# Performance work log

Measured on AMD Instinct MI355X. Metric: run time of the kernel, lower is better.

The kernel has to match this reference:

```python
import jax, jax.numpy as jnp
import numpy as np

K_TOP = 2          # hardcoded k in MyAttentionFunction
S = 32             # hardcoded spatial size (interpolate to 32x32)
N = S * S          # 1024 patches (patch_size=1, stride=1 unfold)
NEG = jnp.float32(-1e30)  # stand-in for excluding columns from top-k


def setup_inputs() -> dict:
    key = jax.random.key(0)
    k1, k2, k3 = jax.random.split(key, 3)
    C = 4096
    generated = jax.random.normal(k1, (1, C, S, S), dtype=jnp.float32)
    known = jax.random.normal(k2, (1, C, S, S), dtype=jnp.float32)
    mask = jax.random.randint(k3, (1, 1, S, S), 0, 2).astype(jnp.float32)
    return {"generated": generated, "known": known, "mask": mask}


def _forward(generated, known, mask):
    C = generated.shape[1]
    # F.interpolate(mask, (32,32)) nearest, then flatten -> flag in {0,1}, shape (N,)
    flag = jax.image.resize(mask, (1, 1, S, S), method="nearest").reshape(N)
    # MyUnfold(x, 1, 1) == [1, N, C]; drop batch dim of 1.
    P = generated.reshape(C, N).T   # (N, C) patches of `generated`
    Kp = known.reshape(C, N).T      # (N, C) patches of `known`

    norm_p = jnp.sum(P * P, axis=-1)   # (N,)
    norm_k = jnp.sum(Kp * Kp, axis=-1)
    # Full cosine matrices; original restricts rows to flag==1 and columns to
    # flag==0 (cosine0) / flag==1 (cosine1) by extraction; we mask columns with
    # a very negative value so top-k returns the same values with GLOBAL indices
    # (which is exactly what the original reconstructs via nonzero()[indexes]).
    cos0 = (P @ Kp.T) / jnp.sqrt(norm_p[:, None] * norm_k[None, :])  # (N, N)
    cos1 = (P @ P.T) / jnp.sqrt(norm_p[:, None] * norm_p[None, :])
    cos0 = jnp.where(flag[None, :] == 0, cos0, NEG)
    cos1 = jnp.where(flag[None, :] == 1, cos1, NEG)

    w0, i0 = jax.lax.top_k(cos0, K_TOP)  # (N, k) values / global indices
    w1, i1 = jax.lax.top_k(cos1, K_TOP)

    m = flag                      # 1.0 on masked rows
    nm = jnp.sum(m)               # number of masked patches
    # weight means taken only over masked rows, then softmax (original uses
    # .item() + numpy softmax, i.e. detached constants).
    means = jnp.stack(
        [jnp.sum(w0[:, i] * m) / nm for i in range(K_TOP)]
        + [jnp.sum(w1[:, i] * m) / nm for i in range(K_TOP)]
    )
    weights = jax.lax.stop_gradient(jax.nn.softmax(means))  # (2k,)

    # The original builds dense 1024x1024 indicator matrices and bmm's them;
    # each indicator row for a masked patch is one-hot at its retrieved source,
    # so the bmm is just a gather into masked rows. The advanced-indexing quirk
    # ind[mask_idx, src_idx] (nonzero() pairs include a leading 0 column) also
    # unconditionally sets ind[0,0]=1; we reproduce that (set semantics: no
    # double count if row 0 already maps to column 0).
    rtn = jnp.zeros((N, C), dtype=generated.dtype)
    for i in range(2 * K_TOP):
        src = Kp if i < K_TOP else P
        cols = (i0 if i < K_TOP else i1)[:, i % K_TOP]  # (N,) global indices
        out_i = jnp.where(m[:, None] == 1, src[cols], 0.0)  # masked rows only
        dup = 1.0 - ((m[0] == 1) & (cols[0] == 0)).astype(src.dtype)
        out_i = out_i.at[0].add(src[0] * dup)  # spurious ind[0,0]=1 artifact
        rtn = rtn + weights[i] * out_i

    rtn = rtn.reshape(1, S, S, C).transpose(0, 3, 1, 2)  # (1, C, 32, 32)
    return jnp.concatenate([generated, known, rtn], axis=1)


def reference(generated, known, mask):
    return _forward(generated, known, mask)
```

## Files before the change

kernel.cpp:

```cpp
#include <hip/hip_runtime.h>
#include <hip/hip_bf16.h>
#include <math.h>

#define N_TOT 1024
#define C_DIM 4096
#define NEGV  -1e30f

typedef __attribute__((ext_vector_type(8))) short short8;
typedef __attribute__((ext_vector_type(4))) float floatx4;

__device__ inline unsigned short bf16_rn(float v) {
    unsigned int u = __float_as_uint(v);
    unsigned int r = (u + 0x7FFFu + ((u >> 16) & 1u)) >> 16;
    return (unsigned short)r;
}

__global__ __launch_bounds__(256) void split_norms(const float* __restrict__ G,
                                                   const float* __restrict__ Kn,
                                                   unsigned short* __restrict__ Phi,
                                                   unsigned short* __restrict__ Plo,
                                                   unsigned short* __restrict__ Khi,
                                                   unsigned short* __restrict__ Klo,
                                                   float* __restrict__ normP,
                                                   float* __restrict__ normK) {
    const int z = blockIdx.z;
    const float* X = z ? Kn : G;
    unsigned short* Xhi = z ? Khi : Phi;
    unsigned short* Xlo = z ? Klo : Plo;
    float* normX = z ? normK : normP;

    __shared__ float tile[64 * 65];
    __shared__ float np[256];
    const int t  = threadIdx.x;
    const int c0 = blockIdx.x * 64;
    const int n0 = blockIdx.y * 64;

    float s2 = 0.0f;
    #pragma unroll
    for (int s = 0; s < 16; s++) {
        int c_loc = s * 4 + (t >> 6);
        int n_loc = t & 63;
        float v = X[(c0 + c_loc) * N_TOT + n0 + n_loc];
        tile[c_loc * 65 + n_loc] = v;
        s2 = fmaf(v, v, s2);
    }
    np[t] = s2;
    __syncthreads();

    if (t < 64) {
        float tot = np[t] + np[t + 64] + np[t + 128] + np[t + 192];
        atomicAdd(&normX[n0 + t], tot);
    }

    #pragma unroll
    for (int s = 0; s < 8; s++) {
        int n_loc = s * 8 + (t >> 5);
        int c2    = (t & 31) * 2;
        float v0 = tile[c2 * 65 + n_loc];
        float v1 = tile[(c2 + 1) * 65 + n_loc];
        unsigned short h0 = bf16_rn(v0);
        unsigned short h1 = bf16_rn(v1);
        float hf0 = __uint_as_float(((unsigned int)h0) << 16);
        float hf1 = __uint_as_float(((unsigned int)h1) << 16);
        unsigned short l0 = bf16_rn(v0 - hf0);
        unsigned short l1 = bf16_rn(v1 - hf1);
        size_t base = (size_t)(n0 + n_loc) * C_DIM + c0 + c2;
        *(ushort2*)&Xhi[base] = make_ushort2(h0, h1);
        *(ushort2*)&Xlo[base] = make_ushort2(l0, l1);
    }
}

__global__ __launch_bounds__(256) void gemm_fused(const unsigned short* __restrict__ Phi,
                                                  const unsigned short* __restrict__ Plo,
                                                  const unsigned short* __restrict__ Khi,
                                                  const unsigned short* __restrict__ Klo,
                                                  float* __restrict__ dot0,
                                                  float* __restrict__ dot1) {
    __shared__ unsigned short sAh[64 * 64];
    __shared__ unsigned short sAl[64 * 64];
    __shared__ unsigned short sKh[64 * 64];
    __shared__ unsigned short sKl[64 * 64];
    __shared__ unsigned short sPh[64 * 64];
    __shared__ unsigned short sPl[64 * 64];

    const int t    = threadIdx.x;
    const int wave = t >> 6, lane = t & 63;
    const int wm   = wave >> 1, wn = wave & 1;
    const int quad = lane >> 4, lrow = lane & 15;
    const int ib = blockIdx.x * 64, jb = blockIdx.y * 64;
    const int k_beg = blockIdx.z * 2048;

    const int srow = t >> 3;
    const int g    = (t & 7) ^ (srow & 7);

    const unsigned short* gAh = Phi + (size_t)(ib + srow) * C_DIM + g * 8;
    const unsigned short* gAl = Plo + (size_t)(ib + srow) * C_DIM + g * 8;
    const unsigned short* gKh = Khi + (size_t)(jb + srow) * C_DIM + g * 8;
    const unsigned short* gKl = Klo + (size_t)(jb + srow) * C_DIM + g * 8;
    const unsigned short* gPh = Phi + (size_t)(jb + srow) * C_DIM + g * 8;
    const unsigned short* gPl = Plo + (size_t)(jb + srow) * C_DIM + g * 8;
    const size_t rstep = (size_t)32 * C_DIM;

    floatx4 acc0[2][2] = {};
    floatx4 acc1[2][2] = {};

    for (int k0 = k_beg; k0 < k_beg + 2048; k0 += 64) {
        #pragma unroll
        for (int q = 0; q < 2; q++) {
            int lds_off = q * 4096 + t * 16;
            #define STAGE(SPTR, GPTR) \
                __builtin_amdgcn_global_load_lds( \
                    (const __attribute__((address_space(1))) void*)((GPTR) + q * rstep + k0), \
                    (__attribute__((address_space(3))) void*)((char*)(SPTR) + lds_off), 16, 0, 0)
            STAGE(sAh, gAh); STAGE(sAl, gAl);
            STAGE(sKh, gKh); STAGE(sKl, gKl);
            STAGE(sPh, gPh); STAGE(sPl, gPl);
            #undef STAGE
        }
        __syncthreads();

        #pragma unroll
        for (int kk = 0; kk < 2; kk++) {
            short8 a_h[2], a_l[2], bk_h[2], bk_l[2], bp_h[2], bp_l[2];
            #pragma unroll
            for (int ti = 0; ti < 2; ti++) {
                int m  = wm * 32 + ti * 16 + lrow;
                int gk = kk * 4 + quad;
                int off = m * 64 + ((gk ^ (m & 7)) << 3);
                a_h[ti] = *(const short8*)&sAh[off];
                a_l[ti] = *(const short8*)&sAl[off];
            }
            #pragma unroll
            for (int tj = 0; tj < 2; tj++) {
                int n  = wn * 32 + tj * 16 + lrow;
                int gk = kk * 4 + quad;
                int off = n * 64 + ((gk ^ (n & 7)) << 3);
                bk_h[tj] = *(const short8*)&sKh[off];
                bk_l[tj] = *(const short8*)&sKl[off];
                bp_h[tj] = *(const short8*)&sPh[off];
                bp_l[tj] = *(const short8*)&sPl[off];
            }
            #pragma unroll
            for (int ti = 0; ti < 2; ti++)
                #pragma unroll
                for (int tj = 0; tj < 2; tj++) {
                    acc0[ti][tj] = __builtin_amdgcn_mfma_f32_16x16x32_bf16(a_h[ti], bk_h[tj], acc0[ti][tj], 0, 0, 0);
                    acc0[ti][tj] = __builtin_amdgcn_mfma_f32_16x16x32_bf16(a_h[ti], bk_l[tj], acc0[ti][tj], 0, 0, 0);
                    acc0[ti][tj] = __builtin_amdgcn_mfma_f32_16x16x32_bf16(a_l[ti], bk_h[tj], acc0[ti][tj], 0, 0, 0);
                    acc1[ti][tj] = __builtin_amdgcn_mfma_f32_16x16x32_bf16(a_h[ti], bp_h[tj], acc1[ti][tj], 0, 0, 0);
                    acc1[ti][tj] = __builtin_amdgcn_mfma_f32_16x16x32_bf16(a_h[ti], bp_l[tj], acc1[ti][tj], 0, 0, 0);
                    acc1[ti][tj] = __builtin_amdgcn_mfma_f32_16x16x32_bf16(a_l[ti], bp_h[tj], acc1[ti][tj], 0, 0, 0);
                }
        }
        __syncthreads();
    }

    #pragma unroll
    for (int tj = 0; tj < 2; tj++) {
        int j = jb + wn * 32 + tj * 16 + lrow;
        #pragma unroll
        for (int ti = 0; ti < 2; ti++) {
            #pragma unroll
            for (int reg = 0; reg < 4; reg++) {
                int i = ib + wm * 32 + ti * 16 + quad * 4 + reg;
                atomicAdd(&dot0[i * N_TOT + j], acc0[ti][tj][reg]);
                atomicAdd(&dot1[i * N_TOT + j], acc1[ti][tj][reg]);
            }
        }
    }
}

__global__ __launch_bounds__(64) void topk_kernel(const float* __restrict__ dot0,
                                                  const float* __restrict__ dot1,
                                                  const float* __restrict__ normP,
                                                  const float* __restrict__ normK,
                                                  const float* __restrict__ flag,
                                                  float* __restrict__ w01,
                                                  int* __restrict__ i01) {
    const int row = blockIdx.x;
    const int z   = blockIdx.y;
    const float* D  = z ? dot1 : dot0;
    const float* nB = z ? normP : normK;
    const float target = z ? 1.0f : 0.0f;
    const int lane = threadIdx.x;
    const float nr = normP[row];

    float v1 = -INFINITY, v2 = -INFINITY;
    int   j1 = -1, j2 = -1;

    for (int s = 0; s < 16; s++) {
        int j = s * 64 + lane;
        float f = flag[j];
        float v = (f == target) ? D[row * N_TOT + j] * rsqrtf(nr * nB[j]) : NEGV;
        if (v > v1 || (v == v1 && j < j1)) {
            v2 = v1; j2 = j1; v1 = v; j1 = j;
        } else if (v > v2 || (v == v2 && j < j2)) {
            v2 = v; j2 = j;
        }
    }

    for (int off = 32; off > 0; off >>= 1) {
        float ov1 = __shfl_down(v1, off);
        float ov2 = __shfl_down(v2, off);
        int   oj1 = __shfl_down(j1, off);
        int   oj2 = __shfl_down(j2, off);
        bool b1 = (ov1 > v1) || (ov1 == v1 && oj1 < j1);
        if (b1) {
            bool b2 = (v1 > ov2) || (v1 == ov2 && j1 < oj2);
            float nv2 = b2 ? v1 : ov2;
            int   nj2 = b2 ? j1 : oj2;
            v1 = ov1; j1 = oj1; v2 = nv2; j2 = nj2;
        } else {
            bool b2 = (ov1 > v2) || (ov1 == v2 && oj1 < j2);
            if (b2) { v2 = ov1; j2 = oj1; }
        }
    }

    if (lane == 0) {
        int base = (z * N_TOT + row) * 2;
        w01[base]     = v1;
        w01[base + 1] = v2;
        i01[base]     = j1;
        i01[base + 1] = j2;
    }
}

__global__ __launch_bounds__(256) void means_kernel(const float* __restrict__ flag,
                                                    const float* __restrict__ w01,
                                                    float* __restrict__ weights) {
    __shared__ float sd[5][256];
    const int t = threadIdx.x;
    float nm = 0.0f, s0 = 0.0f, s1 = 0.0f, s2 = 0.0f, s3 = 0.0f;
    for (int n = t; n < N_TOT; n += 256) {
        float m = flag[n];
        nm += m;
        s0 += m * w01[n * 2 + 0];
        s1 += m * w01[n * 2 + 1];
        s2 += m * w01[2 * N_TOT + n * 2 + 0];
        s3 += m * w01[2 * N_TOT + n * 2 + 1];
    }
    sd[0][t] = nm; sd[1][t] = s0; sd[2][t] = s1; sd[3][t] = s2; sd[4][t] = s3;
    __syncthreads();
    for (int off = 128; off > 0; off >>= 1) {
        if (t < off) {
            #pragma unroll
            for (int q = 0; q < 5; q++) sd[q][t] += sd[q][t + off];
        }
        __syncthreads();
    }
    if (t == 0) {
        float inv = 1.0f / sd[0][0];
        float mv[4] = {sd[1][0] * inv, sd[2][0] * inv, sd[3][0] * inv, sd[4][0] * inv};
        float mx = fmaxf(fmaxf(mv[0], mv[1]), fmaxf(mv[2], mv[3]));
        float e[4], tot = 0.0f;
        #pragma unroll
        for (int q = 0; q < 4; q++) { e[q] = expf(mv[q] - mx); tot += e[q]; }
        #pragma unroll
        for (int q = 0; q < 4; q++) weights[q] = e[q] / tot;
    }
}

__global__ __launch_bounds__(256) void output_kernel(const float* __restrict__ G,
                                                     const float* __restrict__ Kn,
                                                     const float* __restrict__ flag,
                                                     const int* __restrict__ i01,
                                                     const float* __restrict__ weights,
                                                     float* __restrict__ out) {
    const int c  = blockIdx.x;
    const int n4 = threadIdx.x * 4;

    float4 gv = *(const float4*)&G[c * N_TOT + n4];
    float4 kv = *(const float4*)&Kn[c * N_TOT + n4];
    *(float4*)&out[c * N_TOT + n4] = gv;
    *(float4*)&out[C_DIM * N_TOT + c * N_TOT + n4] = kv;

    const float w0 = weights[0], w1 = weights[1], w2 = weights[2], w3 = weights[3];
    float4 fv = *(const float4*)&flag[n4];
    const float fa[4] = {fv.x, fv.y, fv.z, fv.w};

    float val[4];
    #pragma unroll
    for (int e = 0; e < 4; e++) {
        int n = n4 + e;
        float v = 0.0f;
        if (fa[e] == 1.0f) {
            int c00 = i01[n * 2 + 0];
            int c01 = i01[n * 2 + 1];
            int c10 = i01[2 * N_TOT + n * 2 + 0];
            int c11 = i01[2 * N_TOT + n * 2 + 1];
            v = w0 * Kn[c * N_TOT + c00] + w1 * Kn[c * N_TOT + c01]
              + w2 * G[c * N_TOT + c10]  + w3 * G[c * N_TOT + c11];
        }
        if (n == 0) {
            bool m0 = (flag[0] == 1.0f);
            int c00 = i01[0], c01 = i01[1];
            int c10 = i01[2 * N_TOT], c11 = i01[2 * N_TOT + 1];
            float kn0 = Kn[c * N_TOT];
            float g0  = G[c * N_TOT];
            if (!(m0 && c00 == 0)) v += w0 * kn0;
            if (!(m0 && c01 == 0)) v += w1 * kn0;
            if (!(m0 && c10 == 0)) v += w2 * g0;
            if (!(m0 && c11 == 0)) v += w3 * g0;
        }
        val[e] = v;
    }
    *(float4*)&out[2 * C_DIM * N_TOT + c * N_TOT + n4] =
        make_float4(val[0], val[1], val[2], val[3]);
}

extern "C" void kernel_launch(void* const* d_in, const int* in_sizes, int n_in,
                              void* d_out, int out_size, void* d_ws, size_t ws_size,
                              hipStream_t stream) {
    const float* G    = (const float*)d_in[0];
    const float* Kn   = (const float*)d_in[1];
    const float* flag = (const float*)d_in[2];
    float* out = (float*)d_out;

    unsigned short* Phi = (unsigned short*)d_ws;
    unsigned short* Plo = Phi + (size_t)N_TOT * C_DIM;
    unsigned short* Khi = Plo + (size_t)N_TOT * C_DIM;
    unsigned short* Klo = Khi + (size_t)N_TOT * C_DIM;
    float* dot0  = (float*)(Klo + (size_t)N_TOT * C_DIM);
    float* dot1  = dot0 + (size_t)N_TOT * N_TOT;
    float* normP = dot1 + (size_t)N_TOT * N_TOT;
    float* normK = normP + N_TOT;
    float* w01   = normK + N_TOT;
    int*   i01   = (int*)(w01 + 4 * N_TOT);
    float* weights = (float*)(i01 + 4 * N_TOT);

    const size_t zero_bytes = ((size_t)2 * N_TOT * N_TOT + 2 * N_TOT) * sizeof(float);
    hipMemsetAsync(dot0, 0, zero_bytes, stream);

    split_norms<<<dim3(64, 16, 2), 256, 0, stream>>>(G, Kn, Phi, Plo, Khi, Klo, normP, normK);
    gemm_fused<<<dim3(16, 16, 2), 256, 0, stream>>>(Phi, Plo, Khi, Klo, dot0, dot1);
    topk_kernel<<<dim3(1024, 2), 64, 0, stream>>>(dot0, dot1, normP, normK, flag, w01, i01);
    means_kernel<<<1, 256, 0, stream>>>(flag, w01, weights);
    output_kernel<<<4096, 256, 0, stream>>>(G, Kn, flag, i01, weights, out);
}
```

Baseline: 188.2 us.

## Use bf16-only coarse GEMM with top-8 candidate refinement in split precision

The GEMM now computes only hi*hi bf16 products, dropping the lo-part MFMAs and their LDS staging, and splits K four ways. The top-k kernel picks the 8 best candidates per row from the coarse dot products, then recomputes their exact dot products from the hi+lo split and selects the top-2. The means/softmax kernel is folded into every output block, which recomputes the reduction redundantly, and split_norms writes 4-wide vectors. This cuts GEMM MFMA work and LDS traffic by about 3x. The risk is a wrong top-2 if a true neighbor falls outside the coarse top-8, and the output blocks now do duplicated reduction work.

```diff
diff --git a/kernel.cpp b/kernel.cpp
--- a/kernel.cpp
+++ b/kernel.cpp
@@ -4,15 +4,18 @@
 
 #define N_TOT 1024
 #define C_DIM 4096
-#define NEGV  -1e30f
 
 typedef __attribute__((ext_vector_type(8))) short short8;
+typedef __attribute__((ext_vector_type(8))) unsigned short ushort8;
 typedef __attribute__((ext_vector_type(4))) float floatx4;
 
 __device__ inline unsigned short bf16_rn(float v) {
     unsigned int u = __float_as_uint(v);
     unsigned int r = (u + 0x7FFFu + ((u >> 16) & 1u)) >> 16;
     return (unsigned short)r;
+}
+__device__ inline float bf2f(unsigned short h) {
+    return __uint_as_float(((unsigned int)h) << 16);
 }
 
 __global__ __launch_bounds__(256) void split_norms(const float* __restrict__ G,
@@ -53,58 +56,49 @@
     }
 
     #pragma unroll
-    for (int s = 0; s < 8; s++) {
-        int n_loc = s * 8 + (t >> 5);
-        int c2    = (t & 31) * 2;
-        float v0 = tile[c2 * 65 + n_loc];
-        float v1 = tile[(c2 + 1) * 65 + n_loc];
-        unsigned short h0 = bf16_rn(v0);
-        unsigned short h1 = bf16_rn(v1);
-        float hf0 = __uint_as_float(((unsigned int)h0) << 16);
-        float hf1 = __uint_as_float(((unsigned int)h1) << 16);
-        unsigned short l0 = bf16_rn(v0 - hf0);
-        unsigned short l1 = bf16_rn(v1 - hf1);
-        size_t base = (size_t)(n0 + n_loc) * C_DIM + c0 + c2;
-        *(ushort2*)&Xhi[base] = make_ushort2(h0, h1);
-        *(ushort2*)&Xlo[base] = make_ushort2(l0, l1);
-    }
-}
-
-__global__ __launch_bounds__(256) void gemm_fused(const unsigned short* __restrict__ Phi,
-                                                  const unsigned short* __restrict__ Plo,
-                                                  const unsigned short* __restrict__ Khi,
-                                                  const unsigned short* __restrict__ Klo,
-                                                  float* __restrict__ dot0,
-                                                  float* __restrict__ dot1) {
+    for (int s = 0; s < 4; s++) {
+        int n_loc = s * 16 + (t >> 4);
+        int c4    = (t & 15) * 4;
+        unsigned short h[4], l[4];
+        #pragma unroll
+        for (int e = 0; e < 4; e++) {
+            float v = tile[(c4 + e) * 65 + n_loc];
+            h[e] = bf16_rn(v);
+            l[e] = bf16_rn(v - bf2f(h[e]));
+        }
+        size_t base = (size_t)(n0 + n_loc) * C_DIM + c0 + c4;
+        *(ushort4*)&Xhi[base] = make_ushort4(h[0], h[1], h[2], h[3]);
+        *(ushort4*)&Xlo[base] = make_ushort4(l[0], l[1], l[2], l[3]);
+    }
+}
+
+__global__ __launch_bounds__(256, 4) void gemm_coarse(const unsigned short* __restrict__ Phi,
+                                                      const unsigned short* __restrict__ Khi,
+                                                      float* __restrict__ dot0,
+                                                      float* __restrict__ dot1) {
     __shared__ unsigned short sAh[64 * 64];
-    __shared__ unsigned short sAl[64 * 64];
     __shared__ unsigned short sKh[64 * 64];
-    __shared__ unsigned short sKl[64 * 64];
     __shared__ unsigned short sPh[64 * 64];
-    __shared__ unsigned short sPl[64 * 64];
 
     const int t    = threadIdx.x;
     const int wave = t >> 6, lane = t & 63;
     const int wm   = wave >> 1, wn = wave & 1;
     const int quad = lane >> 4, lrow = lane & 15;
     const int ib = blockIdx.x * 64, jb = blockIdx.y * 64;
-    const int k_beg = blockIdx.z * 2048;
+    const int k_beg = blockIdx.z * 1024;
 
     const int srow = t >> 3;
     const int g    = (t & 7) ^ (srow & 7);
 
     const unsigned short* gAh = Phi + (size_t)(ib + srow) * C_DIM + g * 8;
-    const unsigned short* gAl = Plo + (size_t)(ib + srow) * C_DIM + g * 8;
     const unsigned short* gKh = Khi + (size_t)(jb + srow) * C_DIM + g * 8;
-    const unsigned short* gKl = Klo + (size_t)(jb + srow) * C_DIM + g * 8;
     const unsigned short* gPh = Phi + (size_t)(jb + srow) * C_DIM + g * 8;
-    const unsigned short* gPl = Plo + (size_t)(jb + srow) * C_DIM + g * 8;
     const size_t rstep = (size_t)32 * C_DIM;
 
     floatx4 acc0[2][2] = {};
     floatx4 acc1[2][2] = {};
 
-    for (int k0 = k_beg; k0 < k_beg + 2048; k0 += 64) {
+    for (int k0 = k_beg; k0 < k_beg + 1024; k0 += 64) {
         #pragma unroll
         for (int q = 0; q < 2; q++) {
             int lds_off = q * 4096 + t * 16;
@@ -112,23 +106,20 @@
                 __builtin_amdgcn_global_load_lds( \
                     (const __attribute__((address_space(1))) void*)((GPTR) + q * rstep + k0), \
                     (__attribute__((address_space(3))) void*)((char*)(SPTR) + lds_off), 16, 0, 0)
-            STAGE(sAh, gAh); STAGE(sAl, gAl);
-            STAGE(sKh, gKh); STAGE(sKl, gKl);
-            STAGE(sPh, gPh); STAGE(sPl, gPl);
+            STAGE(sAh, gAh); STAGE(sKh, gKh); STAGE(sPh, gPh);
             #undef STAGE
         }
         __syncthreads();
 
         #pragma unroll
         for (int kk = 0; kk < 2; kk++) {
-            short8 a_h[2], a_l[2], bk_h[2], bk_l[2], bp_h[2], bp_l[2];
+            short8 a_h[2], bk_h[2], bp_h[2];
             #pragma unroll
             for (int ti = 0; ti < 2; ti++) {
                 int m  = wm * 32 + ti * 16 + lrow;
                 int gk = kk * 4 + quad;
                 int off = m * 64 + ((gk ^ (m & 7)) << 3);
                 a_h[ti] = *(const short8*)&sAh[off];
-                a_l[ti] = *(const short8*)&sAl[off];
             }
             #pragma unroll
             for (int tj = 0; tj < 2; tj++) {
@@ -136,20 +127,14 @@
                 int gk = kk * 4 + quad;
                 int off = n * 64 + ((gk ^ (n & 7)) << 3);
                 bk_h[tj] = *(const short8*)&sKh[off];
-                bk_l[tj] = *(const short8*)&sKl[off];
                 bp_h[tj] = *(const short8*)&sPh[off];
-                bp_l[tj] = *(const short8*)&sPl[off];
             }
             #pragma unroll
             for (int ti = 0; ti < 2; ti++)
                 #pragma unroll
                 for (int tj = 0; tj < 2; tj++) {
                     acc0[ti][tj] = __builtin_amdgcn_mfma_f32_16x16x32_bf16(a_h[ti], bk_h[tj], acc0[ti][tj], 0, 0, 0);
-                    acc0[ti][tj] = __builtin_amdgcn_mfma_f32_16x16x32_bf16(a_h[ti], bk_l[tj], acc0[ti][tj], 0, 0, 0);
-                    acc0[ti][tj] = __builtin_amdgcn_mfma_f32_16x16x32_bf16(a_l[ti], bk_h[tj], acc0[ti][tj], 0, 0, 0);
                     acc1[ti][tj] = __builtin_amdgcn_mfma_f32_16x16x32_bf16(a_h[ti], bp_h[tj], acc1[ti][tj], 0, 0, 0);
-                    acc1[ti][tj] = __builtin_amdgcn_mfma_f32_16x16x32_bf16(a_h[ti], bp_l[tj], acc1[ti][tj], 0, 0, 0);
-                    acc1[ti][tj] = __builtin_amdgcn_mfma_f32_16x16x32_bf16(a_l[ti], bp_h[tj], acc1[ti][tj], 0, 0, 0);
                 }
         }
         __syncthreads();
@@ -170,8 +155,12 @@
     }
 }
 
-__global__ __launch_bounds__(64) void topk_kernel(const float* __restrict__ dot0,
+__global__ __launch_bounds__(64) void topk_refine(const float* __restrict__ dot0,
                                                   const float* __restrict__ dot1,
+                                                  const unsigned short* __restrict__ Phi,
+                                                  const unsigned short* __restrict__ Plo,
+                                                  const unsigned short* __restrict__ Khi,
+                                                  const unsigned short* __restrict__ Klo,
                                                   const float* __restrict__ normP,
                                                   const float* __restrict__ normK,
                                                   const float* __restrict__ flag,
@@ -179,44 +168,80 @@
                                                   int* __restrict__ i01) {
     const int row = blockIdx.x;
     const int z   = blockIdx.y;
-    const float* D  = z ? dot1 : dot0;
-    const float* nB = z ? normP : normK;
+    const int lane = threadIdx.x;
+    const float* D = z ? dot1 : dot0;
+    const unsigned short* Bh = z ? Phi : Khi;
+    const unsigned short* Bl = z ? Plo : Klo;
     const float target = z ? 1.0f : 0.0f;
-    const int lane = threadIdx.x;
-    const float nr = normP[row];
-
-    float v1 = -INFINITY, v2 = -INFINITY;
-    int   j1 = -1, j2 = -1;
-
+
+    float v[16];
+    #pragma unroll
     for (int s = 0; s < 16; s++) {
         int j = s * 64 + lane;
-        float f = flag[j];
-        float v = (f == target) ? D[row * N_TOT + j] * rsqrtf(nr * nB[j]) : NEGV;
-        if (v > v1 || (v == v1 && j < j1)) {
-            v2 = v1; j2 = j1; v1 = v; j1 = j;
-        } else if (v > v2 || (v == v2 && j < j2)) {
-            v2 = v; j2 = j;
-        }
-    }
-
-    for (int off = 32; off > 0; off >>= 1) {
-        float ov1 = __shfl_down(v1, off);
-        float ov2 = __shfl_down(v2, off);
-        int   oj1 = __shfl_down(j1, off);
-        int   oj2 = __shfl_down(j2, off);
-        bool b1 = (ov1 > v1) || (ov1 == v1 && oj1 < j1);
-        if (b1) {
-            bool b2 = (v1 > ov2) || (v1 == ov2 && j1 < oj2);
-            float nv2 = b2 ? v1 : ov2;
-            int   nj2 = b2 ? j1 : oj2;
-            v1 = ov1; j1 = oj1; v2 = nv2; j2 = nj2;
-        } else {
-            bool b2 = (ov1 > v2) || (ov1 == v2 && oj1 < j2);
-            if (b2) { v2 = ov1; j2 = oj1; }
-        }
-    }
+        v[s] = (flag[j] == target) ? D[row * N_TOT + j] : -INFINITY;
+    }
+
+    int cand[8];
+    #pragma unroll
+    for (int q = 0; q < 8; q++) {
+        float bv = -INFINITY; int bj = 0x7FFFFFFF;
+        #pragma unroll
+        for (int s = 0; s < 16; s++) {
+            int j = s * 64 + lane;
+            if (v[s] > bv || (v[s] == bv && j < bj)) { bv = v[s]; bj = j; }
+        }
+        #pragma unroll
+        for (int off = 32; off > 0; off >>= 1) {
+            float ov = __shfl_xor(bv, off);
+            int   oj = __shfl_xor(bj, off);
+            if (ov > bv || (ov == bv && oj < bj)) { bv = ov; bj = oj; }
+        }
+        cand[q] = bj;
+        if (lane == (bj & 63)) v[bj >> 6] = -INFINITY;
+    }
+
+    const unsigned short* Ah = Phi + (size_t)row * C_DIM;
+    const unsigned short* Al = Plo + (size_t)row * C_DIM;
+    float acc[8] = {};
+    for (int it = 0; it < 8; it++) {
+        int cb = it * 512 + lane * 8;
+        ushort8 ah = *(const ushort8*)&Ah[cb];
+        ushort8 al = *(const ushort8*)&Al[cb];
+        float a[8];
+        #pragma unroll
+        for (int e = 0; e < 8; e++) a[e] = bf2f(ah[e]) + bf2f(al[e]);
+        #pragma unroll
+        for (int q = 0; q < 8; q++) {
+            const unsigned short* bh = Bh + (size_t)cand[q] * C_DIM + cb;
+            const unsigned short* bl = Bl + (size_t)cand[q] * C_DIM + cb;
+            ushort8 hb = *(const ushort8*)bh;
+            ushort8 lb = *(const ushort8*)bl;
+            #pragma unroll
+            for (int e = 0; e < 8; e++)
+                acc[q] = fmaf(a[e], bf2f(hb[e]) + bf2f(lb[e]), acc[q]);
+        }
+    }
+    #pragma unroll
+    for (int q = 0; q < 8; q++)
+        #pragma unroll
+        for (int off = 32; off > 0; off >>= 1)
+            acc[q] += __shfl_xor(acc[q], off);
 
     if (lane == 0) {
+        float nr = normP[row];
+        const float* nB = z ? normP : normK;
+        float v1 = -INFINITY, v2 = -INFINITY;
+        int   j1 = 0x7FFFFFFF, j2 = 0x7FFFFFFF;
+        #pragma unroll
+        for (int q = 0; q < 8; q++) {
+            int j = cand[q];
+            float cv = acc[q] * rsqrtf(nr * nB[j]);
+            if (cv > v1 || (cv == v1 && j < j1)) {
+                v2 = v1; j2 = j1; v1 = cv; j1 = j;
+            } else if (cv > v2 || (cv == v2 && j < j2)) {
+                v2 = cv; j2 = j;
+            }
+        }
         int base = (z * N_TOT + row) * 2;
         w01[base]     = v1;
         w01[base + 1] = v2;
@@ -225,58 +250,64 @@
     }
 }
 
-__global__ __launch_bounds__(256) void means_kernel(const float* __restrict__ flag,
-                                                    const float* __restrict__ w01,
-                                                    float* __restrict__ weights) {
-    __shared__ float sd[5][256];
-    const int t = threadIdx.x;
-    float nm = 0.0f, s0 = 0.0f, s1 = 0.0f, s2 = 0.0f, s3 = 0.0f;
-    for (int n = t; n < N_TOT; n += 256) {
-        float m = flag[n];
-        nm += m;
-        s0 += m * w01[n * 2 + 0];
-        s1 += m * w01[n * 2 + 1];
-        s2 += m * w01[2 * N_TOT + n * 2 + 0];
-        s3 += m * w01[2 * N_TOT + n * 2 + 1];
-    }
-    sd[0][t] = nm; sd[1][t] = s0; sd[2][t] = s1; sd[3][t] = s2; sd[4][t] = s3;
-    __syncthreads();
-    for (int off = 128; off > 0; off >>= 1) {
-        if (t < off) {
-            #pragma unroll
-            for (int q = 0; q < 5; q++) sd[q][t] += sd[q][t + off];
-        }
-        __syncthreads();
-    }
-    if (t == 0) {
-        float inv = 1.0f / sd[0][0];
-        float mv[4] = {sd[1][0] * inv, sd[2][0] * inv, sd[3][0] * inv, sd[4][0] * inv};
-        float mx = fmaxf(fmaxf(mv[0], mv[1]), fmaxf(mv[2], mv[3]));
-        float e[4], tot = 0.0f;
-        #pragma unroll
-        for (int q = 0; q < 4; q++) { e[q] = expf(mv[q] - mx); tot += e[q]; }
-        #pragma unroll
-        for (int q = 0; q < 4; q++) weights[q] = e[q] / tot;
-    }
-}
-
 __global__ __launch_bounds__(256) void output_kernel(const float* __restrict__ G,
                                                      const float* __restrict__ Kn,
                                                      const float* __restrict__ flag,
+                                                     const float* __restrict__ w01,
                                                      const int* __restrict__ i01,
-                                                     const float* __restrict__ weights,
                                                      float* __restrict__ out) {
+    __shared__ float red[5][4];
+    __shared__ float wts[4];
     const int c  = blockIdx.x;
-    const int n4 = threadIdx.x * 4;
+    const int t  = threadIdx.x;
+    const int n4 = t * 4;
+
+    float4 fv = *(const float4*)&flag[n4];
+    const float fa[4] = {fv.x, fv.y, fv.z, fv.w};
+
+    float pm[5] = {};
+    #pragma unroll
+    for (int e = 0; e < 4; e++) {
+        int n = n4 + e;
+        float m = fa[e];
+        pm[0] += m;
+        pm[1] += m * w01[n * 2 + 0];
+        pm[2] += m * w01[n * 2 + 1];
+        pm[3] += m * w01[2 * N_TOT + n * 2 + 0];
+        pm[4] += m * w01[2 * N_TOT + n * 2 + 1];
+    }
+    #pragma unroll
+    for (int i = 0; i < 5; i++)
+        #pragma unroll
+        for (int off = 32; off > 0; off >>= 1)
+            pm[i] += __shfl_xor(pm[i], off);
+    const int wave = t >> 6, lane = t & 63;
+    if (lane == 0) {
+        #pragma unroll
+        for (int i = 0; i < 5; i++) red[i][wave] = pm[i];
+    }
+    __syncthreads();
+    if (t == 0) {
+        float tot[5];
+        #pragma unroll
+        for (int i = 0; i < 5; i++)
+            tot[i] = red[i][0] + red[i][1] + red[i][2] + red[i][3];
+        float inv = 1.0f / tot[0];
+        float mv[4] = {tot[1] * inv, tot[2] * inv, tot[3] * inv, tot[4] * inv};
+        float mx = fmaxf(fmaxf(mv[0], mv[1]), fmaxf(mv[2], mv[3]));
+        float e[4], s = 0.0f;
+        #pragma unroll
+        for (int q = 0; q < 4; q++) { e[q] = expf(mv[q] - mx); s += e[q]; }
+        #pragma unroll
+        for (int q = 0; q < 4; q++) wts[q] = e[q] / s;
+    }
+    __syncthreads();
+    const float w0 = wts[0], w1 = wts[1], w2 = wts[2], w3 = wts[3];
 
     float4 gv = *(const float4*)&G[c * N_TOT + n4];
     float4 kv = *(const float4*)&Kn[c * N_TOT + n4];
     *(float4*)&out[c * N_TOT + n4] = gv;
     *(float4*)&out[C_DIM * N_TOT + c * N_TOT + n4] = kv;
-
-    const float w0 = weights[0], w1 = weights[1], w2 = weights[2], w3 = weights[3];
-    float4 fv = *(const float4*)&flag[n4];
-    const float fa[4] = {fv.x, fv.y, fv.z, fv.w};
 
     float val[4];
     #pragma unroll
@@ -326,14 +357,13 @@
     float* normK = normP + N_TOT;
     float* w01   = normK + N_TOT;
     int*   i01   = (int*)(w01 + 4 * N_TOT);
-    float* weights = (float*)(i01 + 4 * N_TOT);
 
     const size_t zero_bytes = ((size_t)2 * N_TOT * N_TOT + 2 * N_TOT) * sizeof(float);
     hipMemsetAsync(dot0, 0, zero_bytes, stream);
 
     split_norms<<<dim3(64, 16, 2), 256, 0, stream>>>(G, Kn, Phi, Plo, Khi, Klo, normP, normK);
-    gemm_fused<<<dim3(16, 16, 2), 256, 0, stream>>>(Phi, Plo, Khi, Klo, dot0, dot1);
-    topk_kernel<<<dim3(1024, 2), 64, 0, stream>>>(dot0, dot1, normP, normK, flag, w01, i01);
-    means_kernel<<<1, 256, 0, stream>>>(flag, w01, weights);
-    output_kernel<<<4096, 256, 0, stream>>>(G, Kn, flag, i01, weights, out);
-}
+    gemm_coarse<<<dim3(16, 16, 4), 256, 0, stream>>>(Phi, Khi, dot0, dot1);
+    topk_refine<<<dim3(1024, 2), 64, 0, stream>>>(dot0, dot1, Phi, Plo, Khi, Klo,
+                                                  normP, normK, flag, w01, i01);
+    output_kernel<<<4096, 256, 0, stream>>>(G, Kn, flag, w01, i01, out);
+}
```

Result: slower. 198.8 us (+5.6%).
